# Kernel optimization log

Hardware: AMD Instinct MI355X
Metric: run time of the kernel (lower is better)

The kernel has to match this reference:

```python
import jax, jax.numpy as jnp
import numpy as np

EMBED = 768
HEADS = 12
B, S = 32, 1024


def setup_inputs() -> dict:
    key = jax.random.key(0)
    k1, k2, k3 = jax.random.split(key, 3)
    scale_in = 1.0 / np.sqrt(EMBED)
    x = jax.random.normal(k1, (B, S, EMBED), dtype=jnp.float32)
    # weights stored [in, out] (transpose of torch Linear layout)
    w_qkv = jax.random.normal(k2, (EMBED, 3 * EMBED), dtype=jnp.float32) * scale_in
    b_qkv = jnp.zeros((3 * EMBED,), dtype=jnp.float32)
    w_o = jax.random.normal(k3, (EMBED, EMBED), dtype=jnp.float32) * scale_in
    b_o = jnp.zeros((EMBED,), dtype=jnp.float32)
    return {"x": x, "w_qkv": w_qkv, "b_qkv": b_qkv, "w_o": w_o, "b_o": b_o}


def reference(x, w_qkv, b_qkv, w_o, b_o):
    Bt, St, E = x.shape
    H = HEADS
    Dh = E // H
    qkv = x @ w_qkv + b_qkv                      # [B, S, 3E]
    qkv = qkv.reshape(Bt, St, H, 3 * Dh)          # [B, S, H, 3Dh]
    q, k, v = jnp.split(qkv, 3, axis=-1)          # each [B, S, H, Dh]
    # NOTE: faithful to source — attention over the HEADS axis per token,
    # scaled by embed_size**-0.5 (not head_dim**-0.5).
    attn = jnp.einsum('bshd,bsgd->bshg', q, k) * (E ** -0.5)  # [B, S, H, H]
    attn = jax.nn.softmax(attn, axis=-1)
    out = jnp.einsum('bshg,bsgd->bshd', attn, v)  # [B, S, H, Dh]
    out = out.reshape(Bt, St, E)
    return out @ w_o + b_o
```

## Files before the change

kernel.cpp:

```cpp
#include <hip/hip_runtime.h>
#include <hip/hip_bf16.h>

#define EMBED 768
#define HEADS 12
#define TOKENS 32768
#define QKVN  (3*EMBED)
#define KDIM  768
#define QK_SCALE 0.03608439182435161f

typedef __attribute__((ext_vector_type(8))) __bf16 bf16x8;
typedef __attribute__((ext_vector_type(4))) __bf16 bf16x4;
typedef __attribute__((ext_vector_type(4))) float  f32x4;

__device__ __forceinline__ void gload_lds16(const void* gptr, void* lptr) {
    __builtin_amdgcn_global_load_lds(
        (const __attribute__((address_space(1))) void*)gptr,
        (__attribute__((address_space(3))) void*)lptr,
        16, 0, 0);
}

__global__ __launch_bounds__(256) void k_cvt_bf16(const float4* __restrict__ src,
                                                  bf16x4* __restrict__ dst, int n4) {
    int i = blockIdx.x * blockDim.x + threadIdx.x;
    int stride = gridDim.x * blockDim.x;
    for (; i < n4; i += stride) {
        float4 f = src[i];
        bf16x4 o;
        o[0] = (__bf16)f.x; o[1] = (__bf16)f.y; o[2] = (__bf16)f.z; o[3] = (__bf16)f.w;
        dst[i] = o;
    }
}

__global__ __launch_bounds__(256) void k_transpose_cvt(const float* __restrict__ src,
                                                       __bf16* __restrict__ dst,
                                                       int R, int C) {
    __shared__ float tile[32][33];
    int c0 = blockIdx.x * 32, r0 = blockIdx.y * 32;
    int tx = threadIdx.x, ty = threadIdx.y;
#pragma unroll
    for (int j = 0; j < 4; j++) {
        int r = r0 + ty + j * 8;
        tile[ty + j * 8][tx] = src[(long)r * C + c0 + tx];
    }
    __syncthreads();
#pragma unroll
    for (int j = 0; j < 4; j++) {
        int c = c0 + ty + j * 8;
        dst[(long)c * R + r0 + tx] = (__bf16)tile[tx][ty + j * 8];
    }
}

template <typename OutT>
__global__ __launch_bounds__(256, 2) void gemm_kt(const __bf16* __restrict__ A,
                                                  const __bf16* __restrict__ Bt,
                                                  const float* __restrict__ bias,
                                                  OutT* __restrict__ C, int N) {
    extern __shared__ char lds[];
    const int tid = threadIdx.x;
    const int w = tid >> 6, lane = tid & 63;
    const int wc = w;
    const int l15 = lane & 15, l16 = lane >> 4;
    const int K = KDIM;

    const int nbx = N >> 8;
    const int nwg = gridDim.x;
    const int cpx = nwg >> 3;
    const int bid = blockIdx.x;
    const int swz = (bid & 7) * cpx + (bid >> 3);
    const int brow = swz / nbx, bcol = swz % nbx;
    const long arow0 = (long)brow * 128;
    const long ncol0 = (long)bcol * 256;

    const int rowS = w * 16 + (lane >> 2);
    const int cgS  = (((lane & 3) ^ ((lane >> 3) & 3)) * 8);
    const int wofs = w * 1024;

    auto stageA = [&](int r, int kt) {
#pragma unroll
        for (int j = 0; j < 2; ++j)
            gload_lds16(A + (arow0 + j * 64 + rowS) * K + kt * 32 + cgS,
                        lds + r * 8192 + j * 4096 + wofs);
    };
    auto stageB = [&](int r, int kt) {
#pragma unroll
        for (int j = 0; j < 4; ++j)
            gload_lds16(Bt + (ncol0 + j * 64 + rowS) * K + kt * 32 + cgS,
                        lds + 24576 + r * 16384 + j * 4096 + wofs);
    };

    const int swz16 = (l16 ^ ((l15 >> 1) & 3)) * 16;
    const int aco = l15 * 64 + swz16;
    const int bco = wc * 4096 + l15 * 64 + swz16;

    f32x4 acc[8][4] = {};

#define VM6 asm volatile("s_waitcnt vmcnt(6)" ::: "memory")
#define VM0 asm volatile("s_waitcnt vmcnt(0)" ::: "memory")
#define KSTEP(R, STAGE, VW) do { \
    bf16x8 af[8], bfv[4]; \
    _Pragma("unroll") for (int mf = 0; mf < 8; ++mf) \
        af[mf] = *(const bf16x8*)(lds + (R) * 8192 + mf * 1024 + aco); \
    _Pragma("unroll") for (int n = 0; n < 4; ++n) \
        bfv[n] = *(const bf16x8*)(lds + 24576 + (R) * 16384 + n * 1024 + bco); \
    STAGE; \
    __builtin_amdgcn_s_barrier(); \
    asm volatile("s_waitcnt lgkmcnt(0)" ::: "memory"); \
    __builtin_amdgcn_sched_barrier(0); \
    __builtin_amdgcn_s_setprio(1); \
    _Pragma("unroll") for (int mf = 0; mf < 8; ++mf) \
        _Pragma("unroll") for (int n = 0; n < 4; ++n) \
            acc[mf][n] = __builtin_amdgcn_mfma_f32_16x16x32_bf16(af[mf], bfv[n], acc[mf][n], 0, 0, 0); \
    __builtin_amdgcn_s_setprio(0); \
    VW; \
    __builtin_amdgcn_s_barrier(); \
    __builtin_amdgcn_sched_barrier(0); \
} while (0)

    stageA(0, 0); stageB(0, 0);
    stageA(1, 1); stageB(1, 1);
    VM6;
    __builtin_amdgcn_s_barrier();
    __builtin_amdgcn_sched_barrier(0);

    for (int t = 0; t < 21; t += 3) {
        KSTEP(0, stageA(2, t + 2); stageB(2, t + 2), VM6);
        KSTEP(1, stageA(0, t + 3); stageB(0, t + 3), VM6);
        KSTEP(2, stageA(1, t + 4); stageB(1, t + 4), VM6);
    }
    KSTEP(0, stageA(2, 23); stageB(2, 23), VM6);
    KSTEP(1, , VM0);
    KSTEP(2, , );
#undef KSTEP
#undef VM6
#undef VM0

#pragma unroll
    for (int mf = 0; mf < 8; ++mf) {
        const int row = (int)arow0 + mf * 16 + l16 * 4;
#pragma unroll
        for (int n = 0; n < 4; ++n) {
            const int col = (int)ncol0 + wc * 64 + n * 16 + l15;
            const float bv = bias[col];
#pragma unroll
            for (int j = 0; j < 4; ++j) {
                C[(long)(row + j) * N + col] = (OutT)(acc[mf][n][j] + bv);
            }
        }
    }
}

#define HPITCH 200
__global__ __launch_bounds__(256) void k_attn(const __bf16* __restrict__ qkv,
                                              __bf16* __restrict__ out) {
    __shared__ __bf16 rows[4][12 * HPITCH];
    __shared__ float wts[4][144];
    const int w = threadIdx.x >> 6, lane = threadIdx.x & 63;
    const long token = (long)blockIdx.x * 4 + w;
    const __bf16* rp = qkv + token * QKVN;
    __bf16* row = rows[w];
    float* wt  = wts[w];

#pragma unroll
    for (int i = 0; i < 4; i++) {
        int c = i * 64 + lane;
        int h = c / 24;
        *(bf16x8*)(row + h * HPITCH + (c * 8 - h * 192)) = *(const bf16x8*)(rp + c * 8);
    }
    if (lane < 32) {
        int c = 256 + lane;
        int h = c / 24;
        *(bf16x8*)(row + h * HPITCH + (c * 8 - h * 192)) = *(const bf16x8*)(rp + c * 8);
    }
    __syncthreads();

    for (int p = lane; p < 144; p += 64) {
        int h = p / 12, g = p - h * 12;
        const __bf16* qp = row + h * HPITCH;
        const __bf16* kp = row + g * HPITCH + 64;
        float s = 0.f;
#pragma unroll
        for (int d = 0; d < 64; d += 8) {
            bf16x8 qv = *(const bf16x8*)(qp + d);
            bf16x8 kv = *(const bf16x8*)(kp + d);
#pragma unroll
            for (int j = 0; j < 8; j++) s += (float)qv[j] * (float)kv[j];
        }
        wt[p] = s * QK_SCALE;
    }
    __syncthreads();

    if (lane < 12) {
        float s[12];
#pragma unroll
        for (int g = 0; g < 12; g++) s[g] = wt[lane * 12 + g];
        float m = s[0];
#pragma unroll
        for (int g = 1; g < 12; g++) m = fmaxf(m, s[g]);
        float sum = 0.f;
#pragma unroll
        for (int g = 0; g < 12; g++) { s[g] = __expf(s[g] - m); sum += s[g]; }
        float inv = 1.0f / sum;
#pragma unroll
        for (int g = 0; g < 12; g++) wt[lane * 12 + g] = s[g] * inv;
    }
    __syncthreads();

    float vr[12];
#pragma unroll
    for (int g = 0; g < 12; g++) vr[g] = (float)row[g * HPITCH + 128 + lane];
#pragma unroll
    for (int h = 0; h < 12; h++) {
        float a = 0.f;
#pragma unroll
        for (int g = 0; g < 12; g++) a += wt[h * 12 + g] * vr[g];
        out[token * EMBED + h * 64 + lane] = (__bf16)a;
    }
}

extern "C" void kernel_launch(void* const* d_in, const int* in_sizes, int n_in,
                              void* d_out, int out_size, void* d_ws, size_t ws_size,
                              hipStream_t stream) {
    const float* x     = (const float*)d_in[0];
    const float* w_qkv = (const float*)d_in[1];
    const float* b_qkv = (const float*)d_in[2];
    const float* w_o   = (const float*)d_in[3];
    const float* b_o   = (const float*)d_in[4];
    float* out = (float*)d_out;

    char* ws = (char*)d_ws;
    size_t off = 0;
    auto take = [&](size_t bytes) {
        char* p = ws + off;
        off += (bytes + 255) & ~(size_t)255;
        return p;
    };
    __bf16* wqkvt = (__bf16*)take((size_t)QKVN * EMBED * 2);
    __bf16* wot   = (__bf16*)take((size_t)EMBED * EMBED * 2);
    __bf16* xb    = (__bf16*)take((size_t)TOKENS * EMBED * 2);
    __bf16* qkvb  = (__bf16*)take((size_t)TOKENS * QKVN * 2);
    __bf16* attno = xb;

    static bool attr_done = false;
    if (!attr_done) {
        hipFuncSetAttribute((const void*)gemm_kt<__bf16>,
                            hipFuncAttributeMaxDynamicSharedMemorySize, 131072);
        hipFuncSetAttribute((const void*)gemm_kt<float>,
                            hipFuncAttributeMaxDynamicSharedMemorySize, 131072);
        attr_done = true;
    }

    int n4 = TOKENS * EMBED / 4;
    k_cvt_bf16<<<2048, 256, 0, stream>>>((const float4*)x, (bf16x4*)xb, n4);

    dim3 tb(32, 8);
    k_transpose_cvt<<<dim3(QKVN / 32, EMBED / 32), tb, 0, stream>>>(w_qkv, wqkvt, EMBED, QKVN);
    k_transpose_cvt<<<dim3(EMBED / 32, EMBED / 32), tb, 0, stream>>>(w_o, wot, EMBED, EMBED);

    gemm_kt<__bf16><<<(TOKENS / 128) * (QKVN / 256), 256, 73728, stream>>>(
        xb, wqkvt, b_qkv, qkvb, QKVN);

    k_attn<<<TOKENS / 4, 256, 0, stream>>>(qkvb, attno);

    gemm_kt<float><<<(TOKENS / 128) * (EMBED / 256), 256, 73728, stream>>>(
        attno, wot, b_o, out, EMBED);
}
```

Baseline: 253.9 us.

## Pre-pack weights into MFMA fragment layout and load B directly to registers

Replaces the weight transpose with a pack kernel that writes bf16 weights in the per-lane MFMA B-fragment order, so the GEMM loads B straight from global memory into registers instead of staging it through LDS. A is staged with a K-step of 64 and a three-slot XOR-swizzled LDS ring, which halves the number of K iterations and barriers. Static LDS drops to 48KB. The intent is less LDS traffic and less synchronisation per step. The cost is B register prefetch pressure and global-load latency exposed on the B path.

```diff
diff --git a/kernel.cpp b/kernel.cpp
--- a/kernel.cpp
+++ b/kernel.cpp
@@ -6,6 +6,7 @@
 #define TOKENS 32768
 #define QKVN  (3*EMBED)
 #define KDIM  768
+#define NKT   (KDIM/64)
 #define QK_SCALE 0.03608439182435161f
 
 typedef __attribute__((ext_vector_type(8))) __bf16 bf16x8;
@@ -31,115 +32,119 @@
     }
 }
 
-__global__ __launch_bounds__(256) void k_transpose_cvt(const float* __restrict__ src,
-                                                       __bf16* __restrict__ dst,
-                                                       int R, int C) {
-    __shared__ float tile[32][33];
-    int c0 = blockIdx.x * 32, r0 = blockIdx.y * 32;
-    int tx = threadIdx.x, ty = threadIdx.y;
-#pragma unroll
-    for (int j = 0; j < 4; j++) {
-        int r = r0 + ty + j * 8;
-        tile[ty + j * 8][tx] = src[(long)r * C + c0 + tx];
-    }
-    __syncthreads();
-#pragma unroll
-    for (int j = 0; j < 4; j++) {
-        int c = c0 + ty + j * 8;
-        dst[(long)c * R + r0 + tx] = (__bf16)tile[tx][ty + j * 8];
-    }
+__global__ __launch_bounds__(256) void k_pack_b(const float* __restrict__ w,
+                                                __bf16* __restrict__ BF, int N) {
+    int tid = blockIdx.x * 256 + threadIdx.x;
+    int lane = tid & 63;
+    int rest = tid >> 6;
+    int N16 = N >> 4;
+    int ks = rest & 1;
+    int n16 = (rest >> 1) % N16;
+    int kt = (rest >> 1) / N16;
+    if (kt >= NKT) return;
+    int col = n16 * 16 + (lane & 15);
+    int k0 = kt * 64 + ks * 32 + (lane >> 4) * 8;
+    bf16x8 o;
+#pragma unroll
+    for (int e = 0; e < 8; ++e) o[e] = (__bf16)w[(size_t)(k0 + e) * N + col];
+    *(bf16x8*)(BF + (size_t)tid * 8) = o;
 }
 
 template <typename OutT>
-__global__ __launch_bounds__(256, 2) void gemm_kt(const __bf16* __restrict__ A,
-                                                  const __bf16* __restrict__ Bt,
+__global__ __launch_bounds__(256, 2) void gemm_bl(const __bf16* __restrict__ A,
+                                                  const __bf16* __restrict__ BF,
                                                   const float* __restrict__ bias,
                                                   OutT* __restrict__ C, int N) {
-    extern __shared__ char lds[];
+    __shared__ __align__(1024) char lds[49152];
     const int tid = threadIdx.x;
     const int w = tid >> 6, lane = tid & 63;
-    const int wc = w;
     const int l15 = lane & 15, l16 = lane >> 4;
     const int K = KDIM;
+    const int N16 = N >> 4;
+    const long ktstride = (long)N16 * 1024;
 
     const int nbx = N >> 8;
-    const int nwg = gridDim.x;
-    const int cpx = nwg >> 3;
+    const int cpx = gridDim.x >> 3;
     const int bid = blockIdx.x;
     const int swz = (bid & 7) * cpx + (bid >> 3);
     const int brow = swz / nbx, bcol = swz % nbx;
     const long arow0 = (long)brow * 128;
-    const long ncol0 = (long)bcol * 256;
-
-    const int rowS = w * 16 + (lane >> 2);
-    const int cgS  = (((lane & 3) ^ ((lane >> 3) & 3)) * 8);
-    const int wofs = w * 1024;
-
-    auto stageA = [&](int r, int kt) {
-#pragma unroll
-        for (int j = 0; j < 2; ++j)
-            gload_lds16(A + (arow0 + j * 64 + rowS) * K + kt * 32 + cgS,
-                        lds + r * 8192 + j * 4096 + wofs);
+    const int  ncol0 = bcol * 256;
+
+    const __bf16* Asrc = A + (arow0 + w * 8 + (lane >> 3)) * K
+                           + (((lane & 7) ^ (lane >> 3)) * 8);
+    auto stageA = [&](int slot, int kt) {
+#pragma unroll
+        for (int j = 0; j < 4; ++j)
+            gload_lds16(Asrc + (long)(j * 32) * K + (long)kt * 64,
+                        lds + slot * 16384 + j * 4096 + w * 1024 + lane * 16);
     };
-    auto stageB = [&](int r, int kt) {
-#pragma unroll
-        for (int j = 0; j < 4; ++j)
-            gload_lds16(Bt + (ncol0 + j * 64 + rowS) * K + kt * 32 + cgS,
-                        lds + 24576 + r * 16384 + j * 4096 + wofs);
-    };
-
-    const int swz16 = (l16 ^ ((l15 >> 1) & 3)) * 16;
-    const int aco = l15 * 64 + swz16;
-    const int bco = wc * 4096 + l15 * 64 + swz16;
+
+    const int cA0 = l15 * 128 + (((0 * 4 + l16) ^ (l15 & 7)) * 16);
+    const int cA1 = l15 * 128 + (((1 * 4 + l16) ^ (l15 & 7)) * 16);
+
+    const __bf16* bbase = BF + (size_t)lane * 8 + ((long)(ncol0 >> 4) + w * 4) * 1024;
 
     f32x4 acc[8][4] = {};
-
-#define VM6 asm volatile("s_waitcnt vmcnt(6)" ::: "memory")
-#define VM0 asm volatile("s_waitcnt vmcnt(0)" ::: "memory")
-#define KSTEP(R, STAGE, VW) do { \
-    bf16x8 af[8], bfv[4]; \
-    _Pragma("unroll") for (int mf = 0; mf < 8; ++mf) \
-        af[mf] = *(const bf16x8*)(lds + (R) * 8192 + mf * 1024 + aco); \
+    bf16x8 bfv[8];
+
+#define LOADB(KT, HALF) do { \
     _Pragma("unroll") for (int n = 0; n < 4; ++n) \
-        bfv[n] = *(const bf16x8*)(lds + 24576 + (R) * 16384 + n * 1024 + bco); \
-    STAGE; \
-    __builtin_amdgcn_s_barrier(); \
-    asm volatile("s_waitcnt lgkmcnt(0)" ::: "memory"); \
-    __builtin_amdgcn_sched_barrier(0); \
+        bfv[(HALF) * 4 + n] = *(const bf16x8*)(bbase + (long)(KT) * ktstride + n * 1024 + (HALF) * 512); \
+} while (0)
+
+#define VMW12 asm volatile("s_waitcnt vmcnt(12)" ::: "memory")
+#define VMW8  asm volatile("s_waitcnt vmcnt(8)"  ::: "memory")
+
+#define KSTEP(SLOT, BKT, AKT, VMW, DOBAR) do { \
+    bf16x8 af[16]; \
+    _Pragma("unroll") for (int mf = 0; mf < 8; ++mf) \
+        af[mf] = *(const bf16x8*)(lds + (SLOT) * 16384 + mf * 2048 + cA0); \
+    _Pragma("unroll") for (int mf = 0; mf < 8; ++mf) \
+        af[8 + mf] = *(const bf16x8*)(lds + (SLOT) * 16384 + mf * 2048 + cA1); \
     __builtin_amdgcn_s_setprio(1); \
     _Pragma("unroll") for (int mf = 0; mf < 8; ++mf) \
         _Pragma("unroll") for (int n = 0; n < 4; ++n) \
             acc[mf][n] = __builtin_amdgcn_mfma_f32_16x16x32_bf16(af[mf], bfv[n], acc[mf][n], 0, 0, 0); \
     __builtin_amdgcn_s_setprio(0); \
-    VW; \
-    __builtin_amdgcn_s_barrier(); \
-    __builtin_amdgcn_sched_barrier(0); \
+    if ((BKT) >= 0) LOADB(BKT, 0); \
+    __builtin_amdgcn_s_setprio(1); \
+    _Pragma("unroll") for (int mf = 0; mf < 8; ++mf) \
+        _Pragma("unroll") for (int n = 0; n < 4; ++n) \
+            acc[mf][n] = __builtin_amdgcn_mfma_f32_16x16x32_bf16(af[8 + mf], bfv[4 + n], acc[mf][n], 0, 0, 0); \
+    __builtin_amdgcn_s_setprio(0); \
+    if ((BKT) >= 0) LOADB(BKT, 1); \
+    if ((AKT) >= 0) stageA((AKT) % 3, (AKT)); \
+    VMW; \
+    if (DOBAR) { __builtin_amdgcn_s_barrier(); __builtin_amdgcn_sched_barrier(0); } \
 } while (0)
 
-    stageA(0, 0); stageB(0, 0);
-    stageA(1, 1); stageB(1, 1);
-    VM6;
+    stageA(0, 0);
+    LOADB(0, 0); LOADB(0, 1);
+    asm volatile("s_waitcnt vmcnt(0)" ::: "memory");
+    stageA(1, 1);
     __builtin_amdgcn_s_barrier();
     __builtin_amdgcn_sched_barrier(0);
 
-    for (int t = 0; t < 21; t += 3) {
-        KSTEP(0, stageA(2, t + 2); stageB(2, t + 2), VM6);
-        KSTEP(1, stageA(0, t + 3); stageB(0, t + 3), VM6);
-        KSTEP(2, stageA(1, t + 4); stageB(1, t + 4), VM6);
-    }
-    KSTEP(0, stageA(2, 23); stageB(2, 23), VM6);
-    KSTEP(1, , VM0);
-    KSTEP(2, , );
+    for (int t = 0; t < 9; t += 3) {
+        KSTEP(0, t + 1, t + 2, VMW12, 1);
+        KSTEP(1, t + 2, t + 3, VMW12, 1);
+        KSTEP(2, t + 3, t + 4, VMW12, 1);
+    }
+    KSTEP(0, 10, 11, VMW12, 1);
+    KSTEP(1, 11, -1, VMW8, 1);
+    KSTEP(2, -1, -1, , 0);
 #undef KSTEP
-#undef VM6
-#undef VM0
+#undef LOADB
+#undef VMW12
+#undef VMW8
 
 #pragma unroll
     for (int mf = 0; mf < 8; ++mf) {
         const int row = (int)arow0 + mf * 16 + l16 * 4;
 #pragma unroll
         for (int n = 0; n < 4; ++n) {
-            const int col = (int)ncol0 + wc * 64 + n * 16 + l15;
+            const int col = ncol0 + w * 64 + n * 16 + l15;
             const float bv = bias[col];
 #pragma unroll
             for (int j = 0; j < 4; ++j) {
@@ -234,33 +239,23 @@
         off += (bytes + 255) & ~(size_t)255;
         return p;
     };
-    __bf16* wqkvt = (__bf16*)take((size_t)QKVN * EMBED * 2);
-    __bf16* wot   = (__bf16*)take((size_t)EMBED * EMBED * 2);
+    __bf16* wqkvp = (__bf16*)take((size_t)QKVN * KDIM * 2);
+    __bf16* wop   = (__bf16*)take((size_t)EMBED * KDIM * 2);
     __bf16* xb    = (__bf16*)take((size_t)TOKENS * EMBED * 2);
     __bf16* qkvb  = (__bf16*)take((size_t)TOKENS * QKVN * 2);
     __bf16* attno = xb;
 
-    static bool attr_done = false;
-    if (!attr_done) {
-        hipFuncSetAttribute((const void*)gemm_kt<__bf16>,
-                            hipFuncAttributeMaxDynamicSharedMemorySize, 131072);
-        hipFuncSetAttribute((const void*)gemm_kt<float>,
-                            hipFuncAttributeMaxDynamicSharedMemorySize, 131072);
-        attr_done = true;
-    }
-
     int n4 = TOKENS * EMBED / 4;
     k_cvt_bf16<<<2048, 256, 0, stream>>>((const float4*)x, (bf16x4*)xb, n4);
 
-    dim3 tb(32, 8);
-    k_transpose_cvt<<<dim3(QKVN / 32, EMBED / 32), tb, 0, stream>>>(w_qkv, wqkvt, EMBED, QKVN);
-    k_transpose_cvt<<<dim3(EMBED / 32, EMBED / 32), tb, 0, stream>>>(w_o, wot, EMBED, EMBED);
-
-    gemm_kt<__bf16><<<(TOKENS / 128) * (QKVN / 256), 256, 73728, stream>>>(
-        xb, wqkvt, b_qkv, qkvb, QKVN);
+    k_pack_b<<<(NKT * (QKVN / 16) * 2 * 64) / 256, 256, 0, stream>>>(w_qkv, wqkvp, QKVN);
+    k_pack_b<<<(NKT * (EMBED / 16) * 2 * 64) / 256, 256, 0, stream>>>(w_o, wop, EMBED);
+
+    gemm_bl<__bf16><<<(TOKENS / 128) * (QKVN / 256), 256, 0, stream>>>(
+        xb, wqkvp, b_qkv, qkvb, QKVN);
 
     k_attn<<<TOKENS / 4, 256, 0, stream>>>(qkvb, attno);
 
-    gemm_kt<float><<<(TOKENS / 128) * (EMBED / 256), 256, 73728, stream>>>(
-        attno, wot, b_o, out, EMBED);
-}
+    gemm_bl<float><<<(TOKENS / 128) * (EMBED / 256), 256, 0, stream>>>(
+        attno, wop, b_o, out, EMBED);
+}
```

Result: faster. 237.4 us, median of 5 (-6.5%).
